# Kernel tuning notes

Measured on AMD Instinct MI355X. Metric: run time of the kernel, lower is better.

## Reference

```python
import jax, jax.numpy as jnp
import numpy as np

NEG_INF = -1e30

def _rotary_tables(n_pos, d_k):
    # angular_freq = (1/10000)**linspace(0,1,d_k//4), padded with d_k//4 zeros -> d_k//2 freqs
    freqs = (1.0 / 10000.0) ** jnp.linspace(0.0, 1.0, d_k // 4, dtype=jnp.float32)
    freqs = jnp.concatenate([freqs, jnp.zeros(d_k // 4, dtype=jnp.float32)])  # [d_k//2]
    t = jnp.arange(n_pos, dtype=jnp.float32)
    theta = t[:, None] * freqs[None, :]  # [n_pos, d_k//2]
    return jnp.cos(theta), jnp.sin(theta)

def _apply_rotary(x_bhtd, cos, sin):
    # Faithful to torch source: cos/sin are indexed/broadcast along dim -3,
    # which for [B,H,T,D] input is the HEAD axis (original code's quirk).
    c = cos[None, :, None, :]  # [1,H,1,D/2]
    s = sin[None, :, None, :]
    x1, x2 = jnp.split(x_bhtd, 2, axis=-1)
    y1 = x1 * c + x2 * s
    y2 = -x1 * s + x2 * c
    return jnp.concatenate([y1, y2], axis=-1)

def setup_inputs() -> dict:
    key = jax.random.key(0)
    k1, k2, k3 = jax.random.split(key, 3)
    B, S, D = 4, 2048, 2048
    x = jax.random.normal(k1, (B, S, D), dtype=jnp.float32)
    Wqkv = jax.random.normal(k2, (D, 3 * D), dtype=jnp.float32) * (D ** -0.5)
    Wo = jax.random.normal(k3, (D, D), dtype=jnp.float32) * (D ** -0.5)
    return {"x": x, "Wqkv": Wqkv, "Wo": Wo, "n_heads": 16}

def reference(x, Wqkv, Wo, n_heads):
    B, S, D = x.shape
    H = int(n_heads)
    d_k = D // H
    qkv = (x @ Wqkv).reshape(B, S, 3, H, d_k)
    qkv = jnp.transpose(qkv, (2, 0, 3, 1, 4))  # [3,B,H,S,dk]
    Q, K, V = qkv[0], qkv[1], qkv[2]
    cos, sin = _rotary_tables(H, d_k)  # indexed by head axis, per original code
    Q = _apply_rotary(Q, cos, sin)
    K = _apply_rotary(K, cos, sin)
    scores = jnp.einsum('bhqd,bhkd->bhqk', Q, K) / jnp.sqrt(jnp.float32(d_k))
    causal = jnp.tril(jnp.ones((S, S), dtype=bool))
    scores = jnp.where(causal[None, None, :, :], scores, NEG_INF)
    attn = jax.nn.softmax(scores, axis=-1)
    out = jnp.einsum('bhqk,bhkd->bhqd', attn, V)  # [B,H,S,dk]
    out = jnp.transpose(out, (0, 2, 1, 3)).reshape(B, S, D)
    return out @ Wo
```

## Files before the change

### kernel.cpp

```cpp
#include <hip/hip_runtime.h>

typedef __attribute__((ext_vector_type(8))) short short8;
typedef __attribute__((ext_vector_type(4))) short short4v;
typedef __attribute__((ext_vector_type(4))) float f32x4;

__device__ inline short f2bf(float f) {
    union { float f; unsigned u; } v; v.f = f;
    unsigned r = v.u + 0x7fffu + ((v.u >> 16) & 1u);
    return (short)(r >> 16);
}

__device__ __forceinline__ void gload16(const short* g, short* l) {
    __builtin_amdgcn_global_load_lds(
        (const __attribute__((address_space(1))) unsigned int*)g,
        (__attribute__((address_space(3))) unsigned int*)l, 16, 0, 0);
}

__global__ __launch_bounds__(256) void cvt_f32_to_bf16(const float* __restrict__ in,
                                                       short* __restrict__ out, int n4) {
    int i = blockIdx.x * 256 + threadIdx.x;
    if (i >= n4) return;
    float4 v = ((const float4*)in)[i];
    short4v o;
    o[0] = f2bf(v.x); o[1] = f2bf(v.y); o[2] = f2bf(v.z); o[3] = f2bf(v.w);
    ((short4v*)out)[i] = o;
}

__global__ __launch_bounds__(256) void transpose_to_bf16(const float* __restrict__ in,
                                                         short* __restrict__ out,
                                                         int R, int C) {
    __shared__ short tile[64][66];
    int r0 = blockIdx.x * 64, c0 = blockIdx.y * 64;
    int tid = threadIdx.x;
#pragma unroll
    for (int i = 0; i < 16; i++) {
        int idx = i * 256 + tid;
        int r = idx >> 6, c = idx & 63;
        tile[r][c] = f2bf(in[(size_t)(r0 + r) * C + (c0 + c)]);
    }
    __syncthreads();
#pragma unroll
    for (int i = 0; i < 16; i++) {
        int idx = i * 256 + tid;
        int c = idx >> 6, r = idx & 63;
        out[(size_t)(c0 + c) * R + (r0 + r)] = tile[r][c];
    }
}

template <int EPI>
__global__ __launch_bounds__(512) void gemm256(const short* __restrict__ A,
                                               const short* __restrict__ Bt,
                                               int M, int N, int K,
                                               short* __restrict__ O0, short* __restrict__ O1,
                                               short* __restrict__ O2, float* __restrict__ OF,
                                               float qscale) {
    __shared__ short As[2][2][256 * 32];
    __shared__ short Bs[2][2][256 * 32];
    int tid = threadIdx.x, lane = tid & 63, wid = tid >> 6;
    int wr = wid >> 2, wc = wid & 3;
    int mtn = M >> 8;
    int band = mtn >> 3;
    int bid = blockIdx.x;
    int xcd = bid & 7, kk = bid >> 3;
    int nt = kk / band, gmr = kk % band;
    int mt = xcd * band + gmr;
    int row0 = mt << 8, col0 = nt << 8;
    int t15 = lane & 15, t4 = lane >> 4;
    int NT = K >> 6;

    f32x4 acc[8][4];
#pragma unroll
    for (int m = 0; m < 8; m++)
#pragma unroll
        for (int n = 0; n < 4; n++) acc[m][n] = (f32x4){0.f, 0.f, 0.f, 0.f};

    int sg = (lane & 3) ^ ((lane >> 3) & 3);
    int srw = lane >> 2;
    int ce = t4 ^ ((t15 >> 1) & 3);

    auto stageA = [&](int t, int kh) {
        if (t >= NT) return;
        int kb = (t << 6) + (kh << 5);
        short* dst = &As[t & 1][kh][0];
#pragma unroll
        for (int i = 0; i < 2; i++) {
            int seg = wid * 2 + i;
            int row = seg * 16 + srw;
            gload16(A + (size_t)(row0 + row) * K + kb + sg * 8, dst + seg * 512);
        }
    };
    auto stageB = [&](int t, int kh) {
        if (t >= NT) return;
        int kb = (t << 6) + (kh << 5);
        short* dst = &Bs[t & 1][kh][0];
#pragma unroll
        for (int i = 0; i < 2; i++) {
            int seg = wid * 2 + i;
            int row = seg * 16 + srw;
            gload16(Bt + (size_t)(col0 + row) * K + kb + sg * 8, dst + seg * 512);
        }
    };

    auto lda = [&](int d, int kh, short8 (&af)[8]) {
#pragma unroll
        for (int m = 0; m < 8; m++) {
            int row = wr * 128 + m * 16 + t15;
            af[m] = *(short8*)(&As[d][kh][row * 32 + ce * 8]);
        }
    };
    auto ldb = [&](int d, int kh, short8 (&bf)[4]) {
#pragma unroll
        for (int n = 0; n < 4; n++) {
            int row = wc * 64 + n * 16 + t15;
            bf[n] = *(short8*)(&Bs[d][kh][row * 32 + ce * 8]);
        }
    };

#define MFMA32(AF, BF)                                                               \
    __builtin_amdgcn_s_setprio(1);                                                   \
    _Pragma("unroll")                                                                \
    for (int m_ = 0; m_ < 8; m_++)                                                   \
        _Pragma("unroll")                                                            \
        for (int n_ = 0; n_ < 4; n_++)                                               \
            acc[m_][n_] = __builtin_amdgcn_mfma_f32_16x16x32_bf16(                   \
                AF[m_], BF[n_], acc[m_][n_], 0, 0, 0);                               \
    __builtin_amdgcn_s_setprio(0);

    stageA(0, 0); stageB(0, 0);
    stageA(0, 1); stageB(0, 1);
    asm volatile("s_waitcnt vmcnt(0)" ::: "memory");
    asm volatile("s_barrier" ::: "memory");

    for (int t = 0; t < NT; t++) {
        int d = t & 1;
        short8 af0[8], bf0[4], af1[8], bf1[4];
        lda(d, 0, af0); ldb(d, 0, bf0);
        stageA(t + 1, 0); stageB(t + 1, 0);
        stageA(t + 1, 1); stageB(t + 1, 1);
        MFMA32(af0, bf0);
        lda(d, 1, af1); ldb(d, 1, bf1);
        MFMA32(af1, bf1);
        asm volatile("s_waitcnt vmcnt(0)" ::: "memory");
        asm volatile("s_barrier" ::: "memory");
    }

#undef MFMA32

#pragma unroll
    for (int m = 0; m < 8; m++) {
#pragma unroll
        for (int n = 0; n < 4; n++) {
#pragma unroll
            for (int r = 0; r < 4; r++) {
                float v = acc[m][n][r];
                int gm2 = row0 + wr * 128 + m * 16 + t4 * 4 + r;
                int gn = col0 + wc * 64 + n * 16 + t15;
                if (EPI == 0) {
                    int part = gn >> 11, within = gn & 2047;
                    int h = within >> 7, dk = within & 127;
                    int bb = gm2 >> 11, s = gm2 & 2047;
                    int z = bb * 16 + h;
                    if (part == 0) O0[((size_t)z * 2048 + s) * 128 + dk] = f2bf(v * qscale);
                    else if (part == 1) O1[((size_t)z * 2048 + s) * 128 + dk] = f2bf(v);
                    else O2[((size_t)z * 128 + dk) * 2048 + s] = f2bf(v);
                } else {
                    OF[(size_t)gm2 * N + gn] = v;
                }
            }
        }
    }
}

__global__ __launch_bounds__(512, 4) void attn_fwd(const short* __restrict__ Q,
                                                   const short* __restrict__ Kb,
                                                   const short* __restrict__ Vt,
                                                   short* __restrict__ O) {
    __shared__ short Kls[2][64 * 128];
    __shared__ short Vls[128 * 64];
    __shared__ short Pls[8][16 * 72];
    int tid = threadIdx.x, lane = tid & 63, wid = tid >> 6;
    int bx = blockIdx.x, z = blockIdx.y;
    int pr = bx >> 1, hh = bx & 1;
    int qpan = (wid < 4) ? pr : (15 - pr);
    int t15 = lane & 15, t4 = lane >> 4;
    const short* Qh = Q + (size_t)z * 2048 * 128;
    const short* Kh = Kb + (size_t)z * 2048 * 128;
    const short* Vh = Vt + (size_t)z * 128 * 2048;
    int q0w = qpan * 128 + hh * 64 + (wid & 3) * 16;

    short8 qf[4];
    {
        const short* qrow = Qh + (size_t)(q0w + t15) * 128;
#pragma unroll
        for (int s = 0; s < 4; s++) qf[s] = *(const short8*)(qrow + s * 32 + t4 * 8);
    }

    f32x4 o[8];
#pragma unroll
    for (int st = 0; st < 8; st++) o[st] = (f32x4){0.f, 0.f, 0.f, 0.f};
    float m_r[4], l_r[4];
#pragma unroll
    for (int r = 0; r < 4; r++) { m_r[r] = -1e30f; l_r[r] = 0.f; }

    auto stageK = [&](int t, int buf) {
#pragma unroll
        for (int i = 0; i < 2; i++) {
            int seg = wid * 2 + i;
            int row = seg * 4 + t4;
            int kl = (lane & 15) ^ (row & 7);
            gload16(Kh + (size_t)(t * 64 + row) * 128 + kl * 8, &Kls[buf][seg * 512]);
        }
    };
    auto stageV = [&](int t) {
#pragma unroll
        for (int i = 0; i < 2; i++) {
            int seg = wid * 2 + i;
            int row = seg * 8 + (lane >> 3);
            int kl = (lane & 7) ^ (row & 7);
            gload16(Vh + (size_t)row * 2048 + t * 64 + kl * 8, &Vls[seg * 512]);
        }
    };

    int nt = 2 * (15 - pr) + 2;
    stageK(0, 0);
    __syncthreads();

    for (int t = 0; t < nt; t++) {
        int buf = t & 1;
        stageV(t);
        if (t + 1 < nt) stageK(t + 1, buf ^ 1);
        bool active = (t * 64 <= q0w + 15);

        if (active) {
            f32x4 sc[4];
#pragma unroll
            for (int c = 0; c < 4; c++) {
                sc[c] = (f32x4){0.f, 0.f, 0.f, 0.f};
#pragma unroll
                for (int s = 0; s < 4; s++) {
                    int row = c * 16 + t15;
                    int ck = (s * 4 + t4) ^ (row & 7);
                    short8 kf = *(short8*)(&Kls[buf][row * 128 + ck * 8]);
                    sc[c] = __builtin_amdgcn_mfma_f32_16x16x32_bf16(qf[s], kf, sc[c], 0, 0, 0);
                }
            }

            if (t * 64 + 63 > q0w) {
#pragma unroll
                for (int c = 0; c < 4; c++)
#pragma unroll
                    for (int r = 0; r < 4; r++) {
                        int kv = t * 64 + c * 16 + t15, qq = q0w + t4 * 4 + r;
                        if (kv > qq) sc[c][r] = -1e30f;
                    }
            }

            float tm[4];
#pragma unroll
            for (int r = 0; r < 4; r++)
                tm[r] = fmaxf(fmaxf(sc[0][r], sc[1][r]), fmaxf(sc[2][r], sc[3][r]));
            bool need = (tm[0] > m_r[0] + 8.f) | (tm[1] > m_r[1] + 8.f) |
                        (tm[2] > m_r[2] + 8.f) | (tm[3] > m_r[3] + 8.f);
            if (__any(need)) {
#pragma unroll
                for (int r = 0; r < 4; r++) {
#pragma unroll
                    for (int msk = 1; msk <= 8; msk <<= 1)
                        tm[r] = fmaxf(tm[r], __shfl_xor(tm[r], msk));
                    float mn = fmaxf(m_r[r], tm[r]);
                    float scf = __expf(m_r[r] - mn);
                    m_r[r] = mn;
                    l_r[r] *= scf;
#pragma unroll
                    for (int st = 0; st < 8; st++) o[st][r] *= scf;
                }
            }
#pragma unroll
            for (int r = 0; r < 4; r++) {
#pragma unroll
                for (int c = 0; c < 4; c++) {
                    float pv = __expf(sc[c][r] - m_r[r]);
                    Pls[wid][(t4 * 4 + r) * 72 + c * 16 + t15] = f2bf(pv);
                    l_r[r] += pv;
                }
            }
        }

        __syncthreads();

        if (active) {
            short8 pa[2];
#pragma unroll
            for (int s2 = 0; s2 < 2; s2++)
                pa[s2] = *(short8*)(&Pls[wid][0] + t15 * 72 + s2 * 32 + t4 * 8);
#pragma unroll
            for (int st = 0; st < 8; st++) {
#pragma unroll
                for (int s2 = 0; s2 < 2; s2++) {
                    int row = st * 16 + t15;
                    int ck = (s2 * 4 + t4) ^ (row & 7);
                    short8 vf = *(short8*)(&Vls[row * 64 + ck * 8]);
                    o[st] = __builtin_amdgcn_mfma_f32_16x16x32_bf16(pa[s2], vf, o[st], 0, 0, 0);
                }
            }
        }

        __syncthreads();
    }

#pragma unroll
    for (int r = 0; r < 4; r++)
#pragma unroll
        for (int msk = 1; msk <= 8; msk <<= 1)
            l_r[r] += __shfl_xor(l_r[r], msk);

    int b = z >> 4, h = z & 15;
#pragma unroll
    for (int st = 0; st < 8; st++)
#pragma unroll
        for (int r = 0; r < 4; r++) {
            int s = q0w + t4 * 4 + r;
            float val = o[st][r] / l_r[r];
            O[((size_t)b * 2048 + s) * 2048 + h * 128 + st * 16 + t15] = f2bf(val);
        }
}

extern "C" void kernel_launch(void* const* d_in, const int* in_sizes, int n_in,
                              void* d_out, int out_size, void* d_ws, size_t ws_size,
                              hipStream_t stream) {
    const float* x = (const float*)d_in[0];
    const float* Wqkv = (const float*)d_in[1];
    const float* Wo = (const float*)d_in[2];

    const int B = 4, S = 2048, D = 2048, DK = 128;
    const int M = B * S;
    const int N1 = 3 * D;
    (void)in_sizes; (void)n_in; (void)out_size; (void)ws_size;

    char* ws = (char*)d_ws;
    size_t off = 0;
    short* x_bf = (short*)(ws + off);   off += (size_t)M * D * 2;
    short* wqkv_t = (short*)(ws + off); off += (size_t)N1 * D * 2;
    short* wo_t = (short*)(ws + off);   off += (size_t)D * D * 2;
    short* Qb = (short*)(ws + off);     off += (size_t)64 * S * DK * 2;
    short* Kb = (short*)(ws + off);     off += (size_t)64 * S * DK * 2;
    short* Vt = (short*)(ws + off);     off += (size_t)64 * S * DK * 2;
    short* Ob = (short*)(ws + off);     off += (size_t)M * D * 2;

    cvt_f32_to_bf16<<<(M * D / 4 + 255) / 256, 256, 0, stream>>>(x, x_bf, M * D / 4);
    transpose_to_bf16<<<dim3(D / 64, N1 / 64, 1), 256, 0, stream>>>(Wqkv, wqkv_t, D, N1);
    transpose_to_bf16<<<dim3(D / 64, D / 64, 1), 256, 0, stream>>>(Wo, wo_t, D, D);
    gemm256<0><<<(M / 256) * (N1 / 256), 512, 0, stream>>>(
        x_bf, wqkv_t, M, N1, D, Qb, Kb, Vt, nullptr, 0.08838834764831845f);
    attn_fwd<<<dim3(16, 64), 512, 0, stream>>>(Qb, Kb, Vt, Ob);
    gemm256<1><<<(M / 256) * (D / 256), 512, 0, stream>>>(
        Ob, wo_t, M, D, D, nullptr, nullptr, nullptr, (float*)d_out, 1.0f);
}
```

Before: 452.2 us.

## Transpose QK^T MFMA so each lane owns one query row, use exp2 softmax

Swaps the MFMA operands so the score tile comes out transposed, which makes each lane hold a single query row. The online-softmax max and sum then need only two cross-lane shuffles instead of four rows of four-step reductions. The log2(e) factor is folded into the Q scale so exp2f can replace __expf. P is packed to bf16 with v_cvt_pk_bf16_f32 and stored into a swizzled 64-wide LDS layout with 8-byte writes. The rescale factors and final row sums must be redistributed to the PV accumulator layout with extra shuffles.

```diff
diff --git a/kernel.cpp b/kernel.cpp
--- a/kernel.cpp
+++ b/kernel.cpp
@@ -177,7 +177,7 @@
                                                    short* __restrict__ O) {
     __shared__ short Kls[2][64 * 128];
     __shared__ short Vls[128 * 64];
-    __shared__ short Pls[8][16 * 72];
+    __shared__ __align__(16) short Pls[8][16 * 64];
     int tid = threadIdx.x, lane = tid & 63, wid = tid >> 6;
     int bx = blockIdx.x, z = blockIdx.y;
     int pr = bx >> 1, hh = bx & 1;
@@ -198,9 +198,7 @@
     f32x4 o[8];
 #pragma unroll
     for (int st = 0; st < 8; st++) o[st] = (f32x4){0.f, 0.f, 0.f, 0.f};
-    float m_r[4], l_r[4];
-#pragma unroll
-    for (int r = 0; r < 4; r++) { m_r[r] = -1e30f; l_r[r] = 0.f; }
+    float m_s = -1e30f, l_s = 0.f;
 
     auto stageK = [&](int t, int buf) {
 #pragma unroll
@@ -241,48 +239,57 @@
                     int row = c * 16 + t15;
                     int ck = (s * 4 + t4) ^ (row & 7);
                     short8 kf = *(short8*)(&Kls[buf][row * 128 + ck * 8]);
-                    sc[c] = __builtin_amdgcn_mfma_f32_16x16x32_bf16(qf[s], kf, sc[c], 0, 0, 0);
+                    sc[c] = __builtin_amdgcn_mfma_f32_16x16x32_bf16(kf, qf[s], sc[c], 0, 0, 0);
                 }
             }
 
             if (t * 64 + 63 > q0w) {
+                int qq = q0w + t15;
 #pragma unroll
                 for (int c = 0; c < 4; c++)
 #pragma unroll
                     for (int r = 0; r < 4; r++) {
-                        int kv = t * 64 + c * 16 + t15, qq = q0w + t4 * 4 + r;
+                        int kv = t * 64 + c * 16 + t4 * 4 + r;
                         if (kv > qq) sc[c][r] = -1e30f;
                     }
             }
 
-            float tm[4];
-#pragma unroll
-            for (int r = 0; r < 4; r++)
-                tm[r] = fmaxf(fmaxf(sc[0][r], sc[1][r]), fmaxf(sc[2][r], sc[3][r]));
-            bool need = (tm[0] > m_r[0] + 8.f) | (tm[1] > m_r[1] + 8.f) |
-                        (tm[2] > m_r[2] + 8.f) | (tm[3] > m_r[3] + 8.f);
+            float tm = fmaxf(fmaxf(fmaxf(sc[0][0], sc[0][1]), fmaxf(sc[0][2], sc[0][3])),
+                             fmaxf(fmaxf(sc[1][0], sc[1][1]), fmaxf(sc[1][2], sc[1][3])));
+            tm = fmaxf(tm, fmaxf(fmaxf(fmaxf(sc[2][0], sc[2][1]), fmaxf(sc[2][2], sc[2][3])),
+                                 fmaxf(fmaxf(sc[3][0], sc[3][1]), fmaxf(sc[3][2], sc[3][3]))));
+            bool need = (tm > m_s + 8.f);
             if (__any(need)) {
-#pragma unroll
-                for (int r = 0; r < 4; r++) {
-#pragma unroll
-                    for (int msk = 1; msk <= 8; msk <<= 1)
-                        tm[r] = fmaxf(tm[r], __shfl_xor(tm[r], msk));
-                    float mn = fmaxf(m_r[r], tm[r]);
-                    float scf = __expf(m_r[r] - mn);
-                    m_r[r] = mn;
-                    l_r[r] *= scf;
-#pragma unroll
-                    for (int st = 0; st < 8; st++) o[st][r] *= scf;
+                tm = fmaxf(tm, __shfl_xor(tm, 16));
+                tm = fmaxf(tm, __shfl_xor(tm, 32));
+                float mn = fmaxf(m_s, tm);
+                float scf = exp2f(m_s - mn);
+                m_s = mn;
+                l_s *= scf;
+                float sr0 = __shfl(scf, t4 * 4 + 0);
+                float sr1 = __shfl(scf, t4 * 4 + 1);
+                float sr2 = __shfl(scf, t4 * 4 + 2);
+                float sr3 = __shfl(scf, t4 * 4 + 3);
+#pragma unroll
+                for (int st = 0; st < 8; st++) {
+                    o[st][0] *= sr0; o[st][1] *= sr1;
+                    o[st][2] *= sr2; o[st][3] *= sr3;
                 }
             }
-#pragma unroll
-            for (int r = 0; r < 4; r++) {
-#pragma unroll
-                for (int c = 0; c < 4; c++) {
-                    float pv = __expf(sc[c][r] - m_r[r]);
-                    Pls[wid][(t4 * 4 + r) * 72 + c * 16 + t15] = f2bf(pv);
-                    l_r[r] += pv;
-                }
+            int t15l = t15 & 7;
+#pragma unroll
+            for (int c = 0; c < 4; c++) {
+                float p0 = exp2f(sc[c][0] - m_s);
+                float p1 = exp2f(sc[c][1] - m_s);
+                float p2 = exp2f(sc[c][2] - m_s);
+                float p3 = exp2f(sc[c][3] - m_s);
+                l_s += (p0 + p1) + (p2 + p3);
+                unsigned u0, u1;
+                asm("v_cvt_pk_bf16_f32 %0, %1, %2" : "=v"(u0) : "v"(p0), "v"(p1));
+                asm("v_cvt_pk_bf16_f32 %0, %1, %2" : "=v"(u1) : "v"(p2), "v"(p3));
+                int ch = (c * 2 + (t4 >> 1)) ^ t15l;
+                uint2 uu; uu.x = u0; uu.y = u1;
+                *(uint2*)((char*)&Pls[wid][0] + t15 * 128 + ch * 16 + (t4 & 1) * 8) = uu;
             }
         }
 
@@ -291,8 +298,10 @@
         if (active) {
             short8 pa[2];
 #pragma unroll
-            for (int s2 = 0; s2 < 2; s2++)
-                pa[s2] = *(short8*)(&Pls[wid][0] + t15 * 72 + s2 * 32 + t4 * 8);
+            for (int s2 = 0; s2 < 2; s2++) {
+                int ch2 = (s2 * 4 + t4) ^ (t15 & 7);
+                pa[s2] = *(short8*)((char*)&Pls[wid][0] + t15 * 128 + ch2 * 16);
+            }
 #pragma unroll
             for (int st = 0; st < 8; st++) {
 #pragma unroll
@@ -308,11 +317,13 @@
         __syncthreads();
     }
 
-#pragma unroll
-    for (int r = 0; r < 4; r++)
-#pragma unroll
-        for (int msk = 1; msk <= 8; msk <<= 1)
-            l_r[r] += __shfl_xor(l_r[r], msk);
+    l_s += __shfl_xor(l_s, 16);
+    l_s += __shfl_xor(l_s, 32);
+    float lr0 = __shfl(l_s, t4 * 4 + 0);
+    float lr1 = __shfl(l_s, t4 * 4 + 1);
+    float lr2 = __shfl(l_s, t4 * 4 + 2);
+    float lr3 = __shfl(l_s, t4 * 4 + 3);
+    float lr[4] = {lr0, lr1, lr2, lr3};
 
     int b = z >> 4, h = z & 15;
 #pragma unroll
@@ -320,7 +331,7 @@
 #pragma unroll
         for (int r = 0; r < 4; r++) {
             int s = q0w + t4 * 4 + r;
-            float val = o[st][r] / l_r[r];
+            float val = o[st][r] / lr[r];
             O[((size_t)b * 2048 + s) * 2048 + h * 128 + st * 16 + t15] = f2bf(val);
         }
 }
@@ -351,7 +362,7 @@
     transpose_to_bf16<<<dim3(D / 64, N1 / 64, 1), 256, 0, stream>>>(Wqkv, wqkv_t, D, N1);
     transpose_to_bf16<<<dim3(D / 64, D / 64, 1), 256, 0, stream>>>(Wo, wo_t, D, D);
     gemm256<0><<<(M / 256) * (N1 / 256), 512, 0, stream>>>(
-        x_bf, wqkv_t, M, N1, D, Qb, Kb, Vt, nullptr, 0.08838834764831845f);
+        x_bf, wqkv_t, M, N1, D, Qb, Kb, Vt, nullptr, 0.12751743553366927f);
     attn_fwd<<<dim3(16, 64), 512, 0, stream>>>(Qb, Kb, Vt, Ob);
     gemm256<1><<<(M / 256) * (D / 256), 512, 0, stream>>>(
         Ob, wo_t, M, D, D, nullptr, nullptr, nullptr, (float*)d_out, 1.0f);
```

After: 452.6 us. About the same (+0.1%).
